# Kernel tuning notes

Hardware: AMD Instinct MI355X
Metric: run time of the kernel (lower is better)

## Reference

```python
import jax, jax.numpy as jnp
import numpy as np


def setup_inputs() -> dict:
    key = jax.random.key(0)
    k_x, k_w, k_s, k_b = jax.random.split(key, 4)
    B, S, D_IN, D_OUT = 8, 2048, 4096, 4096
    x = jax.random.normal(k_x, (B, S, D_IN), dtype=jnp.float32)
    # int8-valued weights stored as int32 (values in [-128, 127])
    quantized_weights = jax.random.randint(k_w, (D_OUT, D_IN), -128, 128, dtype=jnp.int32)
    scales = jax.random.normal(k_s, (D_OUT,), dtype=jnp.float32)
    bias = jax.random.normal(k_b, (D_OUT,), dtype=jnp.float32)
    return {"x": x, "quantized_weights": quantized_weights, "scales": scales, "bias": bias}


def reference(x, quantized_weights, scales, bias):
    # Per-output-channel dequant: W[o, i] = q[o, i] * scales[o]
    dequantized_weight = quantized_weights.astype(x.dtype) * scales[:, None].astype(x.dtype)
    # F.linear: y = x @ W^T + b
    return jnp.einsum('bsi,oi->bso', x, dequantized_weight) + bias.astype(x.dtype)
```

## Files before the change

kernel.cpp:

```cpp
#include <hip/hip_runtime.h>

#define M_DIM 16384
#define N_DIM 4096
#define K_DIM 4096
#define NT 32

typedef __attribute__((ext_vector_type(4))) float f32x4;
typedef __attribute__((ext_vector_type(8))) short bf16x8;
typedef __attribute__((ext_vector_type(4))) int i32x4;

__device__ __forceinline__ short f2bf(float f) {
    unsigned int u = __builtin_bit_cast(unsigned int, f);
    u += 0x7FFFu + ((u >> 16) & 1u);
    return (short)(u >> 16);
}

__global__ __launch_bounds__(256)
void quant_x_kernel(const float* __restrict__ x, char* __restrict__ x8,
                    float* __restrict__ rs) {
    const int row = blockIdx.x;
    const int tid = threadIdx.x;
    const float* xr = x + (size_t)row * K_DIM;
    f32x4 v[4];
    float am = 0.f;
#pragma unroll
    for (int p = 0; p < 4; ++p) {
        v[p] = *(const f32x4*)(xr + p * 1024 + tid * 4);
#pragma unroll
        for (int e = 0; e < 4; ++e) am = fmaxf(am, fabsf(v[p][e]));
    }
#pragma unroll
    for (int off = 32; off >= 1; off >>= 1)
        am = fmaxf(am, __shfl_xor(am, off, 64));
    __shared__ float smax[4];
    if ((tid & 63) == 0) smax[tid >> 6] = am;
    __syncthreads();
    am = fmaxf(fmaxf(smax[0], smax[1]), fmaxf(smax[2], smax[3]));
    const float inv = am > 0.f ? 127.f / am : 0.f;
    if (tid == 0) rs[row] = am / 127.f;
    int* o32 = (int*)(x8 + (size_t)row * K_DIM);
#pragma unroll
    for (int p = 0; p < 4; ++p) {
        const int b0 = (int)rintf(v[p][0] * inv);
        const int b1 = (int)rintf(v[p][1] * inv);
        const int b2 = (int)rintf(v[p][2] * inv);
        const int b3 = (int)rintf(v[p][3] * inv);
        o32[p * 256 + tid] = (b0 & 255) | ((b1 & 255) << 8) | ((b2 & 255) << 16) | ((b3 & 255) << 24);
    }
}

__global__ void quant_w_kernel(const int* __restrict__ q, char* __restrict__ w8, long n) {
    long i = ((long)blockIdx.x * blockDim.x + threadIdx.x) * 16;
    const long stride = (long)gridDim.x * blockDim.x * 16;
    for (; i < n; i += stride) {
        i32x4 o;
#pragma unroll
        for (int j = 0; j < 4; ++j) {
            i32x4 a = *(const i32x4*)(q + i + j * 4);
            o[j] = (a[0] & 255) | ((a[1] & 255) << 8) | ((a[2] & 255) << 16) | ((a[3] & 255) << 24);
        }
        *(i32x4*)(w8 + i) = o;
    }
}

__device__ __forceinline__ void load_lds16(const void* g, void* l) {
    __builtin_amdgcn_global_load_lds((const __attribute__((address_space(1))) void*)g,
                                     (__attribute__((address_space(3))) void*)l, 16, 0, 0);
}

#define BAR() __builtin_amdgcn_s_barrier()
#define VM(n) asm volatile("s_waitcnt vmcnt(" #n ")" ::: "memory")

__global__ __launch_bounds__(512, 2)
void gemm8p_i8(const char* __restrict__ A, const char* __restrict__ Bw,
               const float* __restrict__ rs, const float* __restrict__ scales,
               const float* __restrict__ bias, float* __restrict__ out) {
    __shared__ char lds[2][4][128 * 128];

    const int tid  = threadIdx.x;
    const int lane = tid & 63;
    const int w    = tid >> 6;
    const int wm   = w >> 2;
    const int wn   = w & 3;
    const int lrow = lane & 15;
    const int lkg  = lane >> 4;
    const int sx   = lane & 7;

    const int nwg = gridDim.x;
    const int swz = (blockIdx.x & 7) * (nwg >> 3) + (blockIdx.x >> 3);
    const int bn  = (swz & 15) * 256;
    const int bm  = (swz >> 4) * 256;

    const char* aS[2];
    const char* bS[2];
#pragma unroll
    for (int L = 0; L < 2; ++L) {
        const int c   = L * 512 + tid;
        const int row = c >> 3;
        const int kc  = (c & 7) ^ (row & 7);
        const int mA  = bm + ((row >> 6) << 7) + (row & 63);
        const int nB  = bn + ((row >> 5) << 6) + (row & 31);
        aS[L] = A  + (size_t)mA * K_DIM + kc * 16;
        bS[L] = Bw + (size_t)nB * K_DIM + kc * 16;
    }
    const int wofs = w << 10;

#define STAGE_A(buf, q, kt) do { \
    char* d = &lds[buf][q][wofs]; \
    const long ko = (long)(kt) * 128 + (long)(q) * (64 * (long)K_DIM); \
    load_lds16(aS[0] + ko, d); \
    load_lds16(aS[1] + ko, d + 8192); \
} while (0)

#define STAGE_B(buf, nh, kt) do { \
    char* d = &lds[buf][2 + (nh)][wofs]; \
    const long ko = (long)(kt) * 128 + (long)(nh) * (32 * (long)K_DIM); \
    load_lds16(bS[0] + ko, d); \
    load_lds16(bS[1] + ko, d + 8192); \
} while (0)

    const int aoff = (wm << 6) + lrow;
    const int boff = (wn << 5) + lrow;

#define RD_A(buf, q, sub, ks) \
    (*(const i32x4*)&lds[buf][q][((aoff + (sub) * 16) << 7) + (((((ks) << 2) + lkg) ^ sx) << 4)])
#define RD_B(buf, nh, sub, ks) \
    (*(const i32x4*)&lds[buf][2 + (nh)][((boff + (sub) * 16) << 7) + (((((ks) << 2) + lkg) ^ sx) << 4)])

    i32x4 acc[8][4];
#pragma unroll
    for (int i = 0; i < 8; ++i)
#pragma unroll
        for (int j = 0; j < 4; ++j)
            acc[i][j] = (i32x4){0, 0, 0, 0};

    i32x4 aF[4][2], bF0[2][2], bF1[2][2];

#define LOAD_AF(buf, q) do { \
    _Pragma("unroll") for (int ii = 0; ii < 4; ++ii) { \
        aF[ii][0] = RD_A(buf, q, ii, 0); aF[ii][1] = RD_A(buf, q, ii, 1); } \
} while (0)
#define LOAD_BF(dst, buf, nh) do { \
    _Pragma("unroll") for (int jj = 0; jj < 2; ++jj) { \
        dst[jj][0] = RD_B(buf, nh, jj, 0); dst[jj][1] = RD_B(buf, nh, jj, 1); } \
} while (0)
#define MMA_Q(mh, nh, BREG) do { \
    __builtin_amdgcn_s_setprio(1); \
    _Pragma("unroll") for (int ii = 0; ii < 4; ++ii) \
    _Pragma("unroll") for (int jj = 0; jj < 2; ++jj) \
    _Pragma("unroll") for (int ks = 0; ks < 2; ++ks) \
        acc[(mh) * 4 + ii][(nh) * 2 + jj] = __builtin_amdgcn_mfma_i32_16x16x64_i8( \
            aF[ii][ks], BREG[jj][ks], acc[(mh) * 4 + ii][(nh) * 2 + jj], 0, 0, 0); \
    __builtin_amdgcn_s_setprio(0); \
} while (0)

    STAGE_A(0, 0, 0); STAGE_A(0, 1, 0); STAGE_B(0, 0, 0); STAGE_B(0, 1, 0);
    STAGE_A(1, 0, 1); STAGE_B(1, 0, 1); STAGE_B(1, 1, 1);
    VM(6);
    BAR();

    for (int it = 0; it < NT / 2; ++it) {
        const int kt  = it * 2;
        const bool s2 = (kt + 2 < NT);
        const bool s3 = (kt + 3 < NT);

        LOAD_AF(0, 0); LOAD_BF(bF0, 0, 0);
        STAGE_A(1, 1, kt + 1);
        BAR(); MMA_Q(0, 0, bF0); BAR();
        LOAD_BF(bF1, 0, 1);
        if (s2) STAGE_A(0, 0, kt + 2);
        BAR(); MMA_Q(0, 1, bF1); BAR();
        LOAD_AF(0, 1);
        if (s2) STAGE_B(0, 0, kt + 2);
        BAR(); MMA_Q(1, 0, bF0); BAR();
        if (s2) { STAGE_B(0, 1, kt + 2); VM(6); } else { VM(0); }
        BAR(); MMA_Q(1, 1, bF1); BAR();
        LOAD_AF(1, 0); LOAD_BF(bF0, 1, 0);
        if (s2) STAGE_A(0, 1, kt + 2);
        BAR(); MMA_Q(0, 0, bF0); BAR();
        LOAD_BF(bF1, 1, 1);
        if (s3) STAGE_A(1, 0, kt + 3);
        BAR(); MMA_Q(0, 1, bF1); BAR();
        LOAD_AF(1, 1);
        if (s3) STAGE_B(1, 0, kt + 3);
        BAR(); MMA_Q(1, 0, bF0); BAR();
        if (s3) { STAGE_B(1, 1, kt + 3); VM(6); }
        BAR(); MMA_Q(1, 1, bF1); BAR();
    }

#pragma unroll
    for (int i = 0; i < 8; ++i) {
        const int r0 = bm + (wm << 7) + i * 16 + (lkg << 2);
        const f32x4 rsv = *(const f32x4*)&rs[r0];
#pragma unroll
        for (int j = 0; j < 4; ++j) {
            const int col = bn + (wn << 6) + j * 16 + lrow;
            const float sc = scales[col];
            const float bb = bias[col];
#pragma unroll
            for (int r = 0; r < 4; ++r)
                out[(size_t)(r0 + r) * N_DIM + col] = (float)acc[i][j][r] * (rsv[r] * sc) + bb;
        }
    }
#undef STAGE_A
#undef STAGE_B
#undef RD_A
#undef RD_B
#undef LOAD_AF
#undef LOAD_BF
#undef MMA_Q
}

__global__ __launch_bounds__(256)
void gemm_fallback(const float* __restrict__ Xf, const int* __restrict__ Qw,
                   const float* __restrict__ scales, const float* __restrict__ bias,
                   float* __restrict__ out) {
    __shared__ short a_lds[128 * 64];
    __shared__ short b_lds[128 * 64];
    const int tid  = threadIdx.x;
    const int lane = tid & 63;
    const int wid  = tid >> 6;
    const int wm   = wid >> 1;
    const int wn   = wid & 1;
    const int bn = (blockIdx.x % (N_DIM / 128)) * 128;
    const int bm = (blockIdx.x / (N_DIM / 128)) * 128;
    const int lrow = lane & 15;
    const int lkg  = lane >> 4;

    f32x4 acc[4][4];
#pragma unroll
    for (int i = 0; i < 4; ++i)
#pragma unroll
        for (int j = 0; j < 4; ++j)
            acc[i][j] = (f32x4){0.f, 0.f, 0.f, 0.f};

    for (int k0 = 0; k0 < K_DIM; k0 += 64) {
#pragma unroll
        for (int t = 0; t < 4; ++t) {
            const int ch  = t * 256 + tid;
            const int row = ch >> 3;
            const int kc  = (ch & 7) ^ (row & 7);
            {
                const float* sa = Xf + (size_t)(bm + row) * K_DIM + k0 + kc * 8;
                f32x4 a0 = *(const f32x4*)sa;
                f32x4 a1 = *(const f32x4*)(sa + 4);
                bf16x8 r;
                r[0] = f2bf(a0[0]); r[1] = f2bf(a0[1]); r[2] = f2bf(a0[2]); r[3] = f2bf(a0[3]);
                r[4] = f2bf(a1[0]); r[5] = f2bf(a1[1]); r[6] = f2bf(a1[2]); r[7] = f2bf(a1[3]);
                *(bf16x8*)&a_lds[ch * 8] = r;
            }
            {
                const int* sb = Qw + (size_t)(bn + row) * K_DIM + k0 + kc * 8;
                i32x4 q0 = *(const i32x4*)sb;
                i32x4 q1 = *(const i32x4*)(sb + 4);
                bf16x8 r;
                r[0] = f2bf((float)q0[0]); r[1] = f2bf((float)q0[1]);
                r[2] = f2bf((float)q0[2]); r[3] = f2bf((float)q0[3]);
                r[4] = f2bf((float)q1[0]); r[5] = f2bf((float)q1[1]);
                r[6] = f2bf((float)q1[2]); r[7] = f2bf((float)q1[3]);
                *(bf16x8*)&b_lds[ch * 8] = r;
            }
        }
        __syncthreads();
#pragma unroll
        for (int ks = 0; ks < 2; ++ks) {
            const int kgl = ks * 4 + lkg;
            bf16x8 af[4], bfr[4];
#pragma unroll
            for (int i = 0; i < 4; ++i) {
                const int am = wm * 64 + i * 16 + lrow;
                af[i]  = *(const bf16x8*)&a_lds[am * 64 + ((kgl ^ (am & 7)) << 3)];
                const int bnn = wn * 64 + i * 16 + lrow;
                bfr[i] = *(const bf16x8*)&b_lds[bnn * 64 + ((kgl ^ (bnn & 7)) << 3)];
            }
#pragma unroll
            for (int i = 0; i < 4; ++i)
#pragma unroll
                for (int j = 0; j < 4; ++j)
                    acc[i][j] = __builtin_amdgcn_mfma_f32_16x16x32_bf16(af[i], bfr[j], acc[i][j], 0, 0, 0);
        }
        __syncthreads();
    }
#pragma unroll
    for (int j = 0; j < 4; ++j) {
        const int col = bn + wn * 64 + j * 16 + lrow;
        const float s  = scales[col];
        const float bb = bias[col];
#pragma unroll
        for (int i = 0; i < 4; ++i) {
            const int row0 = bm + wm * 64 + i * 16 + lkg * 4;
#pragma unroll
            for (int r = 0; r < 4; ++r)
                out[(size_t)(row0 + r) * N_DIM + col] = acc[i][j][r] * s + bb;
        }
    }
}

extern "C" void kernel_launch(void* const* d_in, const int* in_sizes, int n_in,
                              void* d_out, int out_size, void* d_ws, size_t ws_size,
                              hipStream_t stream) {
    const float* x      = (const float*)d_in[0];
    const int*   qw     = (const int*)d_in[1];
    const float* scales = (const float*)d_in[2];
    const float* bias   = (const float*)d_in[3];
    float* out = (float*)d_out;

    const size_t x_elems = (size_t)M_DIM * K_DIM;
    const size_t w_elems = (size_t)N_DIM * K_DIM;
    const size_t need    = x_elems + w_elems + M_DIM * sizeof(float);

    if (ws_size >= need) {
        char*  x8 = (char*)d_ws;
        char*  w8 = x8 + x_elems;
        float* rs = (float*)(w8 + w_elems);
        quant_x_kernel<<<M_DIM, 256, 0, stream>>>(x, x8, rs);
        quant_w_kernel<<<2048, 256, 0, stream>>>(qw, w8, (long)w_elems);
        const dim3 grid((M_DIM / 256) * (N_DIM / 256));
        gemm8p_i8<<<grid, 512, 0, stream>>>(x8, w8, rs, scales, bias, out);
    } else {
        const dim3 grid((M_DIM / 128) * (N_DIM / 128));
        gemm_fallback<<<grid, 256, 0, stream>>>(x, qw, scales, bias, out);
    }
}
```

Before: 344.7 us.

## Fuse quantization kernels, peel last GEMM iteration, use nontemporal output stores

Merges the activation and weight quantization kernels into one launch, with extra blocks covering the weight packing, which removes one kernel launch and its tail. The GEMM main loop is turned into 15 unconditional iterations plus a peeled final iteration, so the staging predicates disappear from the hot loop. Output stores become nontemporal to avoid polluting cache with the large fp32 result. The gains are small and the larger unrolled code may cost instruction cache.

```diff
diff --git a/kernel.cpp b/kernel.cpp
--- a/kernel.cpp
+++ b/kernel.cpp
@@ -7,7 +7,7 @@
 
 typedef __attribute__((ext_vector_type(4))) float f32x4;
 typedef __attribute__((ext_vector_type(8))) short bf16x8;
-typedef __attribute__((ext_vector_type(4))) int i32x4;
+typedef __attribute__((ext_vector_type(4))) int   i32x4;
 
 __device__ __forceinline__ short f2bf(float f) {
     unsigned int u = __builtin_bit_cast(unsigned int, f);
@@ -16,50 +16,52 @@
 }
 
 __global__ __launch_bounds__(256)
-void quant_x_kernel(const float* __restrict__ x, char* __restrict__ x8,
-                    float* __restrict__ rs) {
-    const int row = blockIdx.x;
+void quant_kernel(const float* __restrict__ x, const int* __restrict__ q,
+                  char* __restrict__ x8, char* __restrict__ w8,
+                  float* __restrict__ rs) {
     const int tid = threadIdx.x;
-    const float* xr = x + (size_t)row * K_DIM;
-    f32x4 v[4];
-    float am = 0.f;
-#pragma unroll
-    for (int p = 0; p < 4; ++p) {
-        v[p] = *(const f32x4*)(xr + p * 1024 + tid * 4);
-#pragma unroll
-        for (int e = 0; e < 4; ++e) am = fmaxf(am, fabsf(v[p][e]));
-    }
-#pragma unroll
-    for (int off = 32; off >= 1; off >>= 1)
-        am = fmaxf(am, __shfl_xor(am, off, 64));
-    __shared__ float smax[4];
-    if ((tid & 63) == 0) smax[tid >> 6] = am;
-    __syncthreads();
-    am = fmaxf(fmaxf(smax[0], smax[1]), fmaxf(smax[2], smax[3]));
-    const float inv = am > 0.f ? 127.f / am : 0.f;
-    if (tid == 0) rs[row] = am / 127.f;
-    int* o32 = (int*)(x8 + (size_t)row * K_DIM);
-#pragma unroll
-    for (int p = 0; p < 4; ++p) {
-        const int b0 = (int)rintf(v[p][0] * inv);
-        const int b1 = (int)rintf(v[p][1] * inv);
-        const int b2 = (int)rintf(v[p][2] * inv);
-        const int b3 = (int)rintf(v[p][3] * inv);
-        o32[p * 256 + tid] = (b0 & 255) | ((b1 & 255) << 8) | ((b2 & 255) << 16) | ((b3 & 255) << 24);
-    }
-}
-
-__global__ void quant_w_kernel(const int* __restrict__ q, char* __restrict__ w8, long n) {
-    long i = ((long)blockIdx.x * blockDim.x + threadIdx.x) * 16;
-    const long stride = (long)gridDim.x * blockDim.x * 16;
-    for (; i < n; i += stride) {
-        i32x4 o;
-#pragma unroll
-        for (int j = 0; j < 4; ++j) {
-            i32x4 a = *(const i32x4*)(q + i + j * 4);
-            o[j] = (a[0] & 255) | ((a[1] & 255) << 8) | ((a[2] & 255) << 16) | ((a[3] & 255) << 24);
-        }
-        *(i32x4*)(w8 + i) = o;
+    if (blockIdx.x < M_DIM) {
+        const int row = blockIdx.x;
+        const float* xr = x + (size_t)row * K_DIM;
+        f32x4 v[4];
+        float am = 0.f;
+#pragma unroll
+        for (int p = 0; p < 4; ++p) {
+            v[p] = *(const f32x4*)(xr + p * 1024 + tid * 4);
+#pragma unroll
+            for (int e = 0; e < 4; ++e) am = fmaxf(am, fabsf(v[p][e]));
+        }
+#pragma unroll
+        for (int off = 32; off >= 1; off >>= 1)
+            am = fmaxf(am, __shfl_xor(am, off, 64));
+        __shared__ float smax[4];
+        if ((tid & 63) == 0) smax[tid >> 6] = am;
+        __syncthreads();
+        am = fmaxf(fmaxf(smax[0], smax[1]), fmaxf(smax[2], smax[3]));
+        const float inv = am > 0.f ? 127.f / am : 0.f;
+        if (tid == 0) rs[row] = am / 127.f;
+        int* o32 = (int*)(x8 + (size_t)row * K_DIM);
+#pragma unroll
+        for (int p = 0; p < 4; ++p) {
+            const int b0 = (int)rintf(v[p][0] * inv);
+            const int b1 = (int)rintf(v[p][1] * inv);
+            const int b2 = (int)rintf(v[p][2] * inv);
+            const int b3 = (int)rintf(v[p][3] * inv);
+            o32[p * 256 + tid] = (b0 & 255) | ((b1 & 255) << 8) | ((b2 & 255) << 16) | ((b3 & 255) << 24);
+        }
+    } else {
+        const long n = (long)N_DIM * K_DIM;
+        long i = ((long)(blockIdx.x - M_DIM) * 256 + tid) * 16;
+        const long stride = 2048L * 256 * 16;
+        for (; i < n; i += stride) {
+            i32x4 o;
+#pragma unroll
+            for (int j = 0; j < 4; ++j) {
+                i32x4 a = *(const i32x4*)(q + i + j * 4);
+                o[j] = (a[0] & 255) | ((a[1] & 255) << 8) | ((a[2] & 255) << 16) | ((a[3] & 255) << 24);
+            }
+            *(i32x4*)(w8 + i) = o;
+        }
     }
 }
 
@@ -154,39 +156,42 @@
     __builtin_amdgcn_s_setprio(0); \
 } while (0)
 
+#define PHASES(kt, S1, S2, S3, S4, S5, S6, S7, S8, VMA, VMB) do { \
+    LOAD_AF(0, 0); LOAD_BF(bF0, 0, 0); \
+    S1; BAR(); MMA_Q(0, 0, bF0); BAR(); \
+    LOAD_BF(bF1, 0, 1); \
+    S2; BAR(); MMA_Q(0, 1, bF1); BAR(); \
+    LOAD_AF(0, 1); \
+    S3; BAR(); MMA_Q(1, 0, bF0); BAR(); \
+    S4; VMA; BAR(); MMA_Q(1, 1, bF1); BAR(); \
+    LOAD_AF(1, 0); LOAD_BF(bF0, 1, 0); \
+    S5; BAR(); MMA_Q(0, 0, bF0); BAR(); \
+    LOAD_BF(bF1, 1, 1); \
+    S6; BAR(); MMA_Q(0, 1, bF1); BAR(); \
+    LOAD_AF(1, 1); \
+    S7; BAR(); MMA_Q(1, 0, bF0); BAR(); \
+    S8; VMB; BAR(); MMA_Q(1, 1, bF1); BAR(); \
+} while (0)
+
     STAGE_A(0, 0, 0); STAGE_A(0, 1, 0); STAGE_B(0, 0, 0); STAGE_B(0, 1, 0);
     STAGE_A(1, 0, 1); STAGE_B(1, 0, 1); STAGE_B(1, 1, 1);
     VM(6);
     BAR();
 
-    for (int it = 0; it < NT / 2; ++it) {
-        const int kt  = it * 2;
-        const bool s2 = (kt + 2 < NT);
-        const bool s3 = (kt + 3 < NT);
-
-        LOAD_AF(0, 0); LOAD_BF(bF0, 0, 0);
-        STAGE_A(1, 1, kt + 1);
-        BAR(); MMA_Q(0, 0, bF0); BAR();
-        LOAD_BF(bF1, 0, 1);
-        if (s2) STAGE_A(0, 0, kt + 2);
-        BAR(); MMA_Q(0, 1, bF1); BAR();
-        LOAD_AF(0, 1);
-        if (s2) STAGE_B(0, 0, kt + 2);
-        BAR(); MMA_Q(1, 0, bF0); BAR();
-        if (s2) { STAGE_B(0, 1, kt + 2); VM(6); } else { VM(0); }
-        BAR(); MMA_Q(1, 1, bF1); BAR();
-        LOAD_AF(1, 0); LOAD_BF(bF0, 1, 0);
-        if (s2) STAGE_A(0, 1, kt + 2);
-        BAR(); MMA_Q(0, 0, bF0); BAR();
-        LOAD_BF(bF1, 1, 1);
-        if (s3) STAGE_A(1, 0, kt + 3);
-        BAR(); MMA_Q(0, 1, bF1); BAR();
-        LOAD_AF(1, 1);
-        if (s3) STAGE_B(1, 0, kt + 3);
-        BAR(); MMA_Q(1, 0, bF0); BAR();
-        if (s3) { STAGE_B(1, 1, kt + 3); VM(6); }
-        BAR(); MMA_Q(1, 1, bF1); BAR();
-    }
+    for (int it = 0; it < 15; ++it) {
+        const int kt = it * 2;
+        PHASES(kt,
+               STAGE_A(1, 1, kt + 1),
+               STAGE_A(0, 0, kt + 2),
+               STAGE_B(0, 0, kt + 2),
+               STAGE_B(0, 1, kt + 2),
+               STAGE_A(0, 1, kt + 2),
+               STAGE_A(1, 0, kt + 3),
+               STAGE_B(1, 0, kt + 3),
+               STAGE_B(1, 1, kt + 3),
+               VM(6), VM(6));
+    }
+    PHASES(30, STAGE_A(1, 1, 31), , , , , , , , VM(0), );
 
 #pragma unroll
     for (int i = 0; i < 8; ++i) {
@@ -199,7 +204,8 @@
             const float bb = bias[col];
 #pragma unroll
             for (int r = 0; r < 4; ++r)
-                out[(size_t)(r0 + r) * N_DIM + col] = (float)acc[i][j][r] * (rsv[r] * sc) + bb;
+                __builtin_nontemporal_store((float)acc[i][j][r] * (rsv[r] * sc) + bb,
+                                            &out[(size_t)(r0 + r) * N_DIM + col]);
         }
     }
 #undef STAGE_A
@@ -209,6 +215,7 @@
 #undef LOAD_AF
 #undef LOAD_BF
 #undef MMA_Q
+#undef PHASES
 }
 
 __global__ __launch_bounds__(256)
@@ -313,8 +320,7 @@
         char*  x8 = (char*)d_ws;
         char*  w8 = x8 + x_elems;
         float* rs = (float*)(w8 + w_elems);
-        quant_x_kernel<<<M_DIM, 256, 0, stream>>>(x, x8, rs);
-        quant_w_kernel<<<2048, 256, 0, stream>>>(qw, w8, (long)w_elems);
+        quant_kernel<<<M_DIM + 2048, 256, 0, stream>>>(x, qw, x8, w8, rs);
         const dim3 grid((M_DIM / 256) * (N_DIM / 256));
         gemm8p_i8<<<grid, 512, 0, stream>>>(x8, w8, rs, scales, bias, out);
     } else {
```

New measurement: 337.0 us. -2.2%, faster.
